# Optimization experiments

Hardware: AMD Instinct MI355X
Metric: run time of the kernel (lower is better)

The kernel has to match this reference:

```python
import math
import jax, jax.numpy as jnp
import numpy as np


def _alibi_slopes(n):
    def pow2_slopes(n):
        start = 2.0 ** (-(2.0 ** (-(math.log2(n) - 3))))
        return [start * (start ** i) for i in range(n)]
    if math.log2(n).is_integer():
        return pow2_slopes(n)
    cp2 = 2 ** math.floor(math.log2(n))
    return pow2_slopes(cp2) + _alibi_slopes(2 * cp2)[0::2][: n - cp2]


NUM_HEADS = 16


def setup_inputs() -> dict:
    key = jax.random.key(0)
    ks = jax.random.split(key, 5)
    B, S, H = 2, 2048, 2048
    return {
        "hidden_states": jax.random.normal(ks[0], (B, S, H), jnp.float32),
        "w_qkv": jax.random.normal(ks[1], (H, 3 * H), jnp.float32) * (H ** -0.5),
        "b_qkv": jax.random.normal(ks[2], (3 * H,), jnp.float32) * 0.02,
        "w_proj": jax.random.normal(ks[3], (H, H), jnp.float32) * (H ** -0.5),
        "b_proj": jax.random.normal(ks[4], (H,), jnp.float32) * 0.02,
    }


def reference(hidden_states, w_qkv, b_qkv, w_proj, b_proj):
    B, S, H = hidden_states.shape
    nh = NUM_HEADS
    hd = H // nh
    scale = 1.0 / hd  # mup scale_qk_dot_by_d=True -> d^-1 (not d^-0.5)

    qkv = hidden_states @ w_qkv + b_qkv  # [B,S,3H]
    q, k, v = jnp.split(qkv, 3, axis=-1)
    q = q.reshape(B, S, nh, hd)
    k = k.reshape(B, S, nh, hd)
    v = v.reshape(B, S, nh, hd)

    scores = jnp.einsum("bqhd,bkhd->bhqk", q, k) * scale  # [B,nh,S,S]

    slopes = jnp.asarray(_alibi_slopes(nh), dtype=scores.dtype)  # [nh]
    pos = jnp.arange(S)
    rel = (pos[None, :] - pos[:, None]).astype(scores.dtype)  # j - i, <=0 in causal region
    bias = slopes[:, None, None] * rel[None, :, :]  # [nh,S,S]
    causal = pos[None, :] <= pos[:, None]  # [S,S]

    scores = jnp.where(causal[None, None], scores + bias[None], jnp.finfo(scores.dtype).min)
    attn = jax.nn.softmax(scores, axis=-1)

    out = jnp.einsum("bhqk,bkhd->bqhd", attn, v).reshape(B, S, H)
    return out @ w_proj + b_proj
```

## Files before the change

### kernel.cpp

```cpp
#include <hip/hip_runtime.h>
#include <hip/hip_bf16.h>

typedef short bf16x8 __attribute__((ext_vector_type(8)));
typedef float f32x4 __attribute__((ext_vector_type(4)));
typedef float f32x16 __attribute__((ext_vector_type(16)));
typedef unsigned short ushort_t;

#define NH 16
#define HD 128
#define SEQ 2048
#define HID 2048
#define NQKV 6144
#define BATCH 2

__device__ __forceinline__ ushort_t f2bf(float x) {
    unsigned u = __builtin_bit_cast(unsigned, x);
    u = (u + 0x7fffu + ((u >> 16) & 1u)) >> 16;
    return (ushort_t)u;
}

__device__ __forceinline__ unsigned cvtpk(float lo, float hi) {
    unsigned r;
    asm("v_cvt_pk_bf16_f32 %0, %1, %2" : "=v"(r) : "v"(lo), "v"(hi));
    return r;
}

__device__ __forceinline__ void gl2lds16(const ushort_t* g, ushort_t* l) {
    __builtin_amdgcn_global_load_lds(
        (__attribute__((address_space(1))) void*)(g),
        (__attribute__((address_space(3))) void*)(l), 16, 0, 0);
}

__global__ __launch_bounds__(256) void prep_fused(
    const float* __restrict__ hidden, ushort_t* __restrict__ hbf,
    const float* __restrict__ wqkv, ushort_t* __restrict__ wqkvT,
    const float* __restrict__ wproj, ushort_t* __restrict__ wprojT) {
    const int bid = blockIdx.x;
    const int t = threadIdx.x;
    if (bid >= 12288 && bid < 16384) {
        int i = (bid - 12288) * 256 + t;
        float4 a0 = *(const float4*)(hidden + (size_t)i * 8);
        float4 a1 = *(const float4*)(hidden + (size_t)i * 8 + 4);
        union { ushort_t u[8]; uint4 v; } p;
        p.u[0]=f2bf(a0.x); p.u[1]=f2bf(a0.y); p.u[2]=f2bf(a0.z); p.u[3]=f2bf(a0.w);
        p.u[4]=f2bf(a1.x); p.u[5]=f2bf(a1.y); p.u[6]=f2bf(a1.z); p.u[7]=f2bf(a1.w);
        *(uint4*)(hbf + (size_t)i * 8) = p.v;
        return;
    }
    const float* w;
    ushort_t* wT;
    int N, bx, by;
    if (bid < 12288) {
        w = wqkv; wT = wqkvT; N = NQKV;
        bx = bid % 192; by = bid / 192;
    } else {
        int b2 = bid - 16384;
        w = wproj; wT = wprojT; N = HID;
        bx = b2 % 64; by = b2 / 64;
    }
    __shared__ float tile[32][33];
    const int nb = bx * 32, kb = by * 32;
    const int tx = t & 31, ty = t >> 5;
#pragma unroll
    for (int i = 0; i < 4; ++i) {
        int k = kb + ty + i * 8;
        tile[ty + i * 8][tx] = w[(size_t)k * N + nb + tx];
    }
    __syncthreads();
#pragma unroll
    for (int i = 0; i < 4; ++i) {
        int n = nb + ty + i * 8;
        wT[(size_t)n * HID + kb + tx] = f2bf(tile[tx][ty + i * 8]);
    }
}

#define GEMM_KLOOP(A_, BT_)                                                     \
    const int t = threadIdx.x;                                                  \
    const int w = t >> 6, lane = t & 63, lm = lane & 15, lq = lane >> 4;        \
    const int wm = (w >> 1) * 64, wn = (w & 1) * 64;                            \
    const int lrow = lane >> 3, lsw = (lane & 7) ^ lrow;                        \
    f32x4 acc[4][4] = {};                                                       \
    const ushort_t* gA = A_ + (size_t)(mb + w * 32 + lrow) * HID + lsw * 8;     \
    const ushort_t* gB = BT_ + (size_t)(nb + w * 32 + lrow) * HID + lsw * 8;    \
    for (int kb = 0; kb < HID; kb += 64) {                                      \
        __syncthreads();                                                        \
        _Pragma("unroll")                                                       \
        for (int c = 0; c < 4; ++c) {                                           \
            gl2lds16(gA + (size_t)c * 8 * HID + kb, At + (w * 256 + c * 64) * 8); \
            gl2lds16(gB + (size_t)c * 8 * HID + kb, Bt + (w * 256 + c * 64) * 8); \
        }                                                                       \
        __syncthreads();                                                        \
        _Pragma("unroll")                                                       \
        for (int kc = 0; kc < 2; ++kc) {                                        \
            const int slot = (kc * 4 + lq) ^ (lm & 7);                          \
            bf16x8 af[4], bfr[4];                                               \
            _Pragma("unroll")                                                   \
            for (int mt = 0; mt < 4; ++mt)                                      \
                af[mt] = ((const bf16x8*)At)[(wm + mt * 16 + lm) * 8 + slot];   \
            _Pragma("unroll")                                                   \
            for (int nt = 0; nt < 4; ++nt)                                      \
                bfr[nt] = ((const bf16x8*)Bt)[(wn + nt * 16 + lm) * 8 + slot];  \
            _Pragma("unroll")                                                   \
            for (int mt = 0; mt < 4; ++mt)                                      \
                _Pragma("unroll")                                               \
                for (int nt = 0; nt < 4; ++nt)                                  \
                    acc[mt][nt] = __builtin_amdgcn_mfma_f32_16x16x32_bf16(      \
                        af[mt], bfr[nt], acc[mt][nt], 0, 0, 0);                 \
        }                                                                       \
    }

__global__ __launch_bounds__(256) void gemm_qkv(
    const ushort_t* __restrict__ A, const ushort_t* __restrict__ BT,
    const float* __restrict__ bias,
    ushort_t* __restrict__ qbuf, ushort_t* __restrict__ kbuf,
    ushort_t* __restrict__ vTbuf) {
    __shared__ unsigned shbuf[128 * 68];
    ushort_t* At = (ushort_t*)shbuf;
    ushort_t* Bt = At + 128 * 64;
    const int mb = blockIdx.x * 128;
    const int nb = blockIdx.y * 128;
    GEMM_KLOOP(A, BT)

    const int sec = nb >> 11;
    if (sec < 2) {
#pragma unroll
        for (int mt = 0; mt < 4; ++mt)
#pragma unroll
            for (int nt = 0; nt < 4; ++nt)
#pragma unroll
                for (int r = 0; r < 4; ++r) {
                    int m = mb + wm + mt * 16 + lq * 4 + r;
                    int c = nb + wn + nt * 16 + lm;
                    float val = acc[mt][nt][r] + bias[c];
                    int h = (c >> 7) & 15;
                    int d = c & 127;
                    int b = m >> 11, s = m & 2047;
                    size_t bh = (size_t)(b * NH + h);
                    ushort_t* dst = (sec == 0) ? qbuf : kbuf;
                    dst[(bh * SEQ + s) * HD + d] = f2bf(val);
                }
    } else {
        __syncthreads();
        unsigned* T = shbuf;
#pragma unroll
        for (int mt = 0; mt < 4; ++mt)
#pragma unroll
            for (int nt = 0; nt < 4; ++nt) {
                const int cl = wn + nt * 16 + lm;
                const int ml = wm + mt * 16 + lq * 4;
                const float bb = bias[nb + cl];
#pragma unroll
                for (int r = 0; r < 4; r += 2) {
                    unsigned pk = (unsigned)f2bf(acc[mt][nt][r] + bb) |
                                  ((unsigned)f2bf(acc[mt][nt][r + 1] + bb) << 16);
                    T[cl * 68 + ((ml + r) >> 1)] = pk;
                }
            }
        __syncthreads();
        const int d = t & 127, sh = t >> 7;
        const int b = mb >> 11, sbase = mb & 2047;
        const int hv = (nb >> 7) - 32;
        ushort_t* vrow = vTbuf + ((size_t)(b * NH + hv) * HD + d) * SEQ + sbase + sh * 64;
#pragma unroll
        for (int i = 0; i < 8; ++i)
            *(uint4*)(vrow + i * 8) = *(const uint4*)&T[d * 68 + sh * 32 + i * 4];
    }
}

__global__ __launch_bounds__(256) void gemm_proj(
    const ushort_t* __restrict__ A, const ushort_t* __restrict__ BT,
    const float* __restrict__ bias, float* __restrict__ out) {
    __shared__ ushort_t Abuf[128 * 64];
    __shared__ ushort_t Bbuf[128 * 64];
    ushort_t* At = Abuf;
    ushort_t* Bt = Bbuf;
    const int mb = blockIdx.x * 128;
    const int nb = blockIdx.y * 128;
    GEMM_KLOOP(A, BT)
#pragma unroll
    for (int mt = 0; mt < 4; ++mt)
#pragma unroll
        for (int nt = 0; nt < 4; ++nt)
#pragma unroll
            for (int r = 0; r < 4; ++r) {
                int m = mb + wm + mt * 16 + lq * 4 + r;
                int c = nb + wn + nt * 16 + lm;
                out[(size_t)m * HID + c] = acc[mt][nt][r] + bias[c];
            }
}

__global__ __launch_bounds__(256) void attn_kernel(
    const ushort_t* __restrict__ qb, const ushort_t* __restrict__ kbuf,
    const ushort_t* __restrict__ vT, ushort_t* __restrict__ ob) {
    __shared__ ushort_t Ks[64 * 128];
    __shared__ ushort_t Vs[128 * 64];

    const int bid = blockIdx.x;
    const int x = bid & 7, g = bid >> 3;
    const int qt = 15 - (g >> 2);
    const int bh = ((g & 3) << 3) | x;
    const int qbase = qt * 128;
    const int t = threadIdx.x, w = t >> 6, lane = t & 63;
    const int l31 = lane & 31, hl = lane >> 5;

    const ushort_t* Qg = qb + (size_t)bh * SEQ * HD;
    const ushort_t* Kg = kbuf + (size_t)bh * SEQ * HD;
    const ushort_t* Vg = vT + (size_t)bh * HD * SEQ;

    const int h = bh & 15;
    const float LOG2E = 1.44269504f;
    const float slope2 = exp2f(-0.5f * (float)(h + 1)) * LOG2E;
    const float scale2 = (1.0f / 128.0f) * LOG2E;

    const int qrow = qbase + w * 32 + l31;
    const int ktd = (qbase + w * 32 + 31) >> 6;

    bf16x8 qf[8];
#pragma unroll
    for (int s = 0; s < 8; ++s) {
        uint4 qv = *(const uint4*)(Qg + (size_t)qrow * HD + (2 * s + hl) * 8);
        qf[s] = __builtin_bit_cast(bf16x8, qv);
    }

    int koffs[4], voffs[4];
#pragma unroll
    for (int i = 0; i < 4; ++i) {
        int ci = i * 256 + t;
        int kr = ci >> 4, ks = ci & 15;
        int kcg = (ks & 8) | ((ks & 7) ^ (kr & 7));
        koffs[i] = kr * HD + kcg * 8;
        int vr = ci >> 3, vs = ci & 7;
        int vcg = vs ^ (vr & 7);
        voffs[i] = vr * SEQ + vcg * 8;
    }

    float mrow = -1e30f, lrow = 0.0f;
    f32x16 O[4] = {};
    const int nkt = 2 * qt + 2;

    for (int kt = 0; kt < nkt; ++kt) {
        __syncthreads();
        {
            const ushort_t* Kt_ = Kg + (size_t)kt * 64 * HD;
            const ushort_t* Vt_ = Vg + (size_t)kt * 64;
#pragma unroll
            for (int i = 0; i < 4; ++i) {
                gl2lds16(Kt_ + koffs[i], Ks + (i * 256 + w * 64) * 8);
                gl2lds16(Vt_ + voffs[i], Vs + (i * 256 + w * 64) * 8);
            }
        }
        __syncthreads();

        if (kt > ktd) continue;

        f32x16 s0 = {}, s1 = {};
        __builtin_amdgcn_s_setprio(1);
#pragma unroll
        for (int s = 0; s < 8; ++s) {
            const int c = 2 * s + hl;
            const int slot = (c & 8) | ((c & 7) ^ (l31 & 7));
            bf16x8 k0 = *(const bf16x8*)&Ks[(l31 * 16 + slot) * 8];
            bf16x8 k1 = *(const bf16x8*)&Ks[((32 + l31) * 16 + slot) * 8];
            s0 = __builtin_amdgcn_mfma_f32_32x32x16_bf16(k0, qf[s], s0, 0, 0, 0);
            s1 = __builtin_amdgcn_mfma_f32_32x32x16_bf16(k1, qf[s], s1, 0, 0, 0);
        }
        __builtin_amdgcn_s_setprio(0);

        const float sb = slope2 * (float)(kt * 64 + 4 * hl - qrow);
        float tm = -3e38f;
        if (kt == ktd) {
#pragma unroll
            for (int r = 0; r < 16; ++r) {
                const int Cr = (r & 3) + 8 * (r >> 2);
                float v0 = s0[r] * scale2 + (sb + slope2 * (float)Cr);
                float v1 = s1[r] * scale2 + (sb + slope2 * (float)(Cr + 32));
                int k0i = kt * 64 + Cr + 4 * hl;
                v0 = (k0i <= qrow) ? v0 : -3e38f;
                v1 = (k0i + 32 <= qrow) ? v1 : -3e38f;
                s0[r] = v0; s1[r] = v1;
                tm = fmaxf(tm, fmaxf(v0, v1));
            }
        } else {
#pragma unroll
            for (int r = 0; r < 16; ++r) {
                const int Cr = (r & 3) + 8 * (r >> 2);
                float v0 = s0[r] * scale2 + (sb + slope2 * (float)Cr);
                float v1 = s1[r] * scale2 + (sb + slope2 * (float)(Cr + 32));
                s0[r] = v0; s1[r] = v1;
                tm = fmaxf(tm, fmaxf(v0, v1));
            }
        }
        tm = fmaxf(tm, __shfl_xor(tm, 32));

        const bool noresc = __all(tm <= mrow + 8.0f) && (kt > 0);
        float mnew, alpha;
        if (noresc) { mnew = mrow; alpha = 1.0f; }
        else { mnew = fmaxf(mrow, tm); alpha = __builtin_amdgcn_exp2f(mrow - mnew); }
        mrow = mnew;

        float psum = 0.0f;
#pragma unroll
        for (int r = 0; r < 16; ++r) {
            float p0 = __builtin_amdgcn_exp2f(s0[r] - mnew);
            float p1 = __builtin_amdgcn_exp2f(s1[r] - mnew);
            s0[r] = p0; s1[r] = p1;
            psum += p0 + p1;
        }
        psum += __shfl_xor(psum, 32);
        lrow = lrow * alpha + psum;

        if (!noresc) {
#pragma unroll
            for (int dt = 0; dt < 4; ++dt)
#pragma unroll
                for (int r = 0; r < 16; ++r) O[dt][r] *= alpha;
        }

        unsigned c0[8], c1[8];
#pragma unroll
        for (int G = 0; G < 4; ++G) {
            c0[G]     = cvtpk(s0[4 * G + 0], s0[4 * G + 1]);
            c1[G]     = cvtpk(s0[4 * G + 2], s0[4 * G + 3]);
            c0[4 + G] = cvtpk(s1[4 * G + 0], s1[4 * G + 1]);
            c1[4 + G] = cvtpk(s1[4 * G + 2], s1[4 * G + 3]);
        }

        __builtin_amdgcn_s_setprio(1);
#pragma unroll
        for (int ks = 0; ks < 4; ++ks) {
            unsigned a0 = c0[2 * ks], a1 = c1[2 * ks];
            unsigned b0 = c0[2 * ks + 1], b1 = c1[2 * ks + 1];
            unsigned own0 = hl ? b0 : a0, own1 = hl ? b1 : a1;
            unsigned snd0 = hl ? a0 : b0, snd1 = hl ? a1 : b1;
            unsigned rcv0 = __shfl_xor(snd0, 32);
            unsigned rcv1 = __shfl_xor(snd1, 32);
            union { unsigned u[4]; bf16x8 v; } pf;
            pf.u[0] = hl ? rcv0 : own0;
            pf.u[1] = hl ? rcv1 : own1;
            pf.u[2] = hl ? own0 : rcv0;
            pf.u[3] = hl ? own1 : rcv1;
            const int c = 2 * ks + hl;
#pragma unroll
            for (int dt = 0; dt < 4; ++dt) {
                const int vr = dt * 32 + l31;
                const int slot = c ^ (vr & 7);
                bf16x8 vf = *(const bf16x8*)&Vs[(vr * 8 + slot) * 8];
                O[dt] = __builtin_amdgcn_mfma_f32_32x32x16_bf16(vf, pf.v, O[dt], 0, 0, 0);
            }
        }
        __builtin_amdgcn_s_setprio(0);
    }

    const float lb = __builtin_amdgcn_rcpf(lrow);
    const int b = bh >> 4;
    ushort_t* orow = ob + ((size_t)(b * SEQ + qrow)) * HID + h * HD;
#pragma unroll
    for (int dt = 0; dt < 4; ++dt)
#pragma unroll
        for (int g4 = 0; g4 < 4; ++g4) {
            union { ushort_t u[4]; uint2 v; } pk;
            pk.u[0] = f2bf(O[dt][4 * g4 + 0] * lb);
            pk.u[1] = f2bf(O[dt][4 * g4 + 1] * lb);
            pk.u[2] = f2bf(O[dt][4 * g4 + 2] * lb);
            pk.u[3] = f2bf(O[dt][4 * g4 + 3] * lb);
            *(uint2*)(orow + dt * 32 + 8 * g4 + 4 * hl) = pk.v;
        }
}

extern "C" void kernel_launch(void* const* d_in, const int* in_sizes, int n_in,
                              void* d_out, int out_size, void* d_ws, size_t ws_size,
                              hipStream_t stream) {
    const float* hidden = (const float*)d_in[0];
    const float* w_qkv = (const float*)d_in[1];
    const float* b_qkv = (const float*)d_in[2];
    const float* w_proj = (const float*)d_in[3];
    const float* b_proj = (const float*)d_in[4];
    float* out = (float*)d_out;

    char* ws = (char*)d_ws;
    size_t off = 0;
    ushort_t* wqkvT = (ushort_t*)(ws + off); off += (size_t)NQKV * HID * 2;
    ushort_t* wprojT = (ushort_t*)(ws + off); off += (size_t)HID * HID * 2;
    ushort_t* hbf = (ushort_t*)(ws + off); off += (size_t)BATCH * SEQ * HID * 2;
    ushort_t* qw = (ushort_t*)(ws + off); off += (size_t)BATCH * NH * SEQ * HD * 2;
    ushort_t* kw = (ushort_t*)(ws + off); off += (size_t)BATCH * NH * SEQ * HD * 2;
    ushort_t* vTw = (ushort_t*)(ws + off); off += (size_t)BATCH * NH * SEQ * HD * 2;
    ushort_t* attnw = (ushort_t*)(ws + off); off += (size_t)BATCH * SEQ * HID * 2;

    prep_fused<<<dim3(20480), 256, 0, stream>>>(
        hidden, hbf, w_qkv, wqkvT, w_proj, wprojT);

    gemm_qkv<<<dim3(BATCH * SEQ / 128, NQKV / 128), 256, 0, stream>>>(
        hbf, wqkvT, b_qkv, qw, kw, vTw);

    attn_kernel<<<dim3(BATCH * NH * 16), 256, 0, stream>>>(qw, kw, vTw, attnw);

    gemm_proj<<<dim3(BATCH * SEQ / 128, HID / 128), 256, 0, stream>>>(
        attnw, wprojT, b_proj, out);
}
```

Before: 368.6 us.

## Double-buffer K/V tiles in attention kernel to overlap loads with compute

Adds two LDS buffers each for the K and V tiles and prefetches tile kt+1 into the idle buffer while tile kt is computed. Partial vmcnt waits keep the next tile's global-to-LDS copies in flight during compute. This hides load latency behind the MFMA work. In exchange LDS use doubles from 32KB to 64KB per block, which may lower occupancy.

```diff
diff --git a/kernel.cpp b/kernel.cpp
--- a/kernel.cpp
+++ b/kernel.cpp
@@ -192,8 +192,8 @@
 __global__ __launch_bounds__(256) void attn_kernel(
     const ushort_t* __restrict__ qb, const ushort_t* __restrict__ kbuf,
     const ushort_t* __restrict__ vT, ushort_t* __restrict__ ob) {
-    __shared__ ushort_t Ks[64 * 128];
-    __shared__ ushort_t Vs[128 * 64];
+    __shared__ ushort_t Ks[2][64 * 128];
+    __shared__ ushort_t Vs[2][128 * 64];
 
     const int bid = blockIdx.x;
     const int x = bid & 7, g = bid >> 3;
@@ -234,22 +234,34 @@
         voffs[i] = vr * SEQ + vcg * 8;
     }
 
+#define ATTN_STAGE(KT, BUF)                                                   \
+    {                                                                         \
+        const ushort_t* Kt_ = Kg + (size_t)(KT) * 64 * HD;                    \
+        const ushort_t* Vt_ = Vg + (size_t)(KT) * 64;                         \
+        _Pragma("unroll")                                                     \
+        for (int i = 0; i < 4; ++i) {                                         \
+            gl2lds16(Kt_ + koffs[i], Ks[BUF] + (i * 256 + w * 64) * 8);       \
+            gl2lds16(Vt_ + voffs[i], Vs[BUF] + (i * 256 + w * 64) * 8);       \
+        }                                                                     \
+    }
+
     float mrow = -1e30f, lrow = 0.0f;
     f32x16 O[4] = {};
     const int nkt = 2 * qt + 2;
 
+    ATTN_STAGE(0, 0)
+
     for (int kt = 0; kt < nkt; ++kt) {
-        __syncthreads();
-        {
-            const ushort_t* Kt_ = Kg + (size_t)kt * 64 * HD;
-            const ushort_t* Vt_ = Vg + (size_t)kt * 64;
-#pragma unroll
-            for (int i = 0; i < 4; ++i) {
-                gl2lds16(Kt_ + koffs[i], Ks + (i * 256 + w * 64) * 8);
-                gl2lds16(Vt_ + voffs[i], Vs + (i * 256 + w * 64) * 8);
-            }
-        }
-        __syncthreads();
+        const int cur = kt & 1;
+        __builtin_amdgcn_s_barrier();
+        if (kt + 1 < nkt) {
+            ATTN_STAGE(kt + 1, cur ^ 1)
+            asm volatile("s_waitcnt vmcnt(8)" ::: "memory");
+        } else {
+            asm volatile("s_waitcnt vmcnt(0)" ::: "memory");
+        }
+        __builtin_amdgcn_s_barrier();
+        __builtin_amdgcn_sched_barrier(0);
 
         if (kt > ktd) continue;
 
@@ -259,8 +271,8 @@
         for (int s = 0; s < 8; ++s) {
             const int c = 2 * s + hl;
             const int slot = (c & 8) | ((c & 7) ^ (l31 & 7));
-            bf16x8 k0 = *(const bf16x8*)&Ks[(l31 * 16 + slot) * 8];
-            bf16x8 k1 = *(const bf16x8*)&Ks[((32 + l31) * 16 + slot) * 8];
+            bf16x8 k0 = *(const bf16x8*)&Ks[cur][(l31 * 16 + slot) * 8];
+            bf16x8 k1 = *(const bf16x8*)&Ks[cur][((32 + l31) * 16 + slot) * 8];
             s0 = __builtin_amdgcn_mfma_f32_32x32x16_bf16(k0, qf[s], s0, 0, 0, 0);
             s1 = __builtin_amdgcn_mfma_f32_32x32x16_bf16(k1, qf[s], s1, 0, 0, 0);
         }
@@ -344,7 +356,7 @@
             for (int dt = 0; dt < 4; ++dt) {
                 const int vr = dt * 32 + l31;
                 const int slot = c ^ (vr & 7);
-                bf16x8 vf = *(const bf16x8*)&Vs[(vr * 8 + slot) * 8];
+                bf16x8 vf = *(const bf16x8*)&Vs[cur][(vr * 8 + slot) * 8];
                 O[dt] = __builtin_amdgcn_mfma_f32_32x32x16_bf16(vf, pf.v, O[dt], 0, 0, 0);
             }
         }
@@ -365,6 +377,7 @@
             pk.u[3] = f2bf(O[dt][4 * g4 + 3] * lb);
             *(uint2*)(orow + dt * 32 + 8 * g4 + 4 * hl) = pk.v;
         }
+#undef ATTN_STAGE
 }
 
 extern "C" void kernel_launch(void* const* d_in, const int* in_sizes, int n_in,
```

Measured after the change: 371.0 us. No clear change (+0.6%).

## Move w_proj transpose into attention kernel tail and reorder query tiles

Applied to the files above, without the earlier changes.

The w_proj fp32-to-bf16 transpose moves out of the prep kernel and runs as extra blocks appended to the attention launch. These cheap blocks can fill compute units that sit idle during the attention's load-imbalanced tail, and the prep kernel shrinks. The query-tile ordering also changes: the first half of the grid issues long causal tiles in descending order and the second half issues short tiles in ascending order, to improve load balance. The cost is some added branching in the attention kernel, and the transpose reuses the K shared-memory buffer as its tile.

```diff
diff --git a/kernel.cpp b/kernel.cpp
--- a/kernel.cpp
+++ b/kernel.cpp
@@ -33,11 +33,10 @@
 
 __global__ __launch_bounds__(256) void prep_fused(
     const float* __restrict__ hidden, ushort_t* __restrict__ hbf,
-    const float* __restrict__ wqkv, ushort_t* __restrict__ wqkvT,
-    const float* __restrict__ wproj, ushort_t* __restrict__ wprojT) {
+    const float* __restrict__ wqkv, ushort_t* __restrict__ wqkvT) {
     const int bid = blockIdx.x;
     const int t = threadIdx.x;
-    if (bid >= 12288 && bid < 16384) {
+    if (bid >= 12288) {
         int i = (bid - 12288) * 256 + t;
         float4 a0 = *(const float4*)(hidden + (size_t)i * 8);
         float4 a1 = *(const float4*)(hidden + (size_t)i * 8 + 4);
@@ -47,30 +46,20 @@
         *(uint4*)(hbf + (size_t)i * 8) = p.v;
         return;
     }
-    const float* w;
-    ushort_t* wT;
-    int N, bx, by;
-    if (bid < 12288) {
-        w = wqkv; wT = wqkvT; N = NQKV;
-        bx = bid % 192; by = bid / 192;
-    } else {
-        int b2 = bid - 16384;
-        w = wproj; wT = wprojT; N = HID;
-        bx = b2 % 64; by = b2 / 64;
-    }
+    const int bx = bid % 192, by = bid / 192;
     __shared__ float tile[32][33];
     const int nb = bx * 32, kb = by * 32;
     const int tx = t & 31, ty = t >> 5;
 #pragma unroll
     for (int i = 0; i < 4; ++i) {
         int k = kb + ty + i * 8;
-        tile[ty + i * 8][tx] = w[(size_t)k * N + nb + tx];
+        tile[ty + i * 8][tx] = wqkv[(size_t)k * NQKV + nb + tx];
     }
     __syncthreads();
 #pragma unroll
     for (int i = 0; i < 4; ++i) {
         int n = nb + ty + i * 8;
-        wT[(size_t)n * HID + kb + tx] = f2bf(tile[tx][ty + i * 8]);
+        wqkvT[(size_t)n * HID + kb + tx] = f2bf(tile[tx][ty + i * 8]);
     }
 }
 
@@ -189,18 +178,42 @@
             }
 }
 
-__global__ __launch_bounds__(256) void attn_kernel(
+__global__ __launch_bounds__(256) void attn_fused(
     const ushort_t* __restrict__ qb, const ushort_t* __restrict__ kbuf,
-    const ushort_t* __restrict__ vT, ushort_t* __restrict__ ob) {
+    const ushort_t* __restrict__ vT, ushort_t* __restrict__ ob,
+    const float* __restrict__ wproj, ushort_t* __restrict__ wprojT) {
     __shared__ ushort_t Ks[64 * 128];
     __shared__ ushort_t Vs[128 * 64];
 
     const int bid = blockIdx.x;
-    const int x = bid & 7, g = bid >> 3;
-    const int qt = 15 - (g >> 2);
-    const int bh = ((g & 3) << 3) | x;
+    const int t = threadIdx.x;
+
+    if (bid >= 512) {
+        float* tile = (float*)Ks;
+        const int b2 = bid - 512;
+        const int bx = b2 & 63, by = b2 >> 6;
+        const int nb = bx * 32, kb = by * 32;
+        const int tx = t & 31, ty = t >> 5;
+#pragma unroll
+        for (int i = 0; i < 4; ++i) {
+            int k = kb + ty + i * 8;
+            tile[(ty + i * 8) * 33 + tx] = wproj[(size_t)k * HID + nb + tx];
+        }
+        __syncthreads();
+#pragma unroll
+        for (int i = 0; i < 4; ++i) {
+            int n = nb + ty + i * 8;
+            wprojT[(size_t)n * HID + kb + tx] = f2bf(tile[tx * 33 + ty + i * 8]);
+        }
+        return;
+    }
+
+    const int x = bid & 7, j = bid >> 3;
+    const int hi = j & 3, m = j >> 2;
+    const int qt = (m < 8) ? (15 - m) : (m - 8);
+    const int bh = (hi << 3) | x;
     const int qbase = qt * 128;
-    const int t = threadIdx.x, w = t >> 6, lane = t & 63;
+    const int w = t >> 6, lane = t & 63;
     const int l31 = lane & 31, hl = lane >> 5;
 
     const ushort_t* Qg = qb + (size_t)bh * SEQ * HD;
@@ -387,13 +400,13 @@
     ushort_t* vTw = (ushort_t*)(ws + off); off += (size_t)BATCH * NH * SEQ * HD * 2;
     ushort_t* attnw = (ushort_t*)(ws + off); off += (size_t)BATCH * SEQ * HID * 2;
 
-    prep_fused<<<dim3(20480), 256, 0, stream>>>(
-        hidden, hbf, w_qkv, wqkvT, w_proj, wprojT);
+    prep_fused<<<dim3(16384), 256, 0, stream>>>(hidden, hbf, w_qkv, wqkvT);
 
     gemm_qkv<<<dim3(BATCH * SEQ / 128, NQKV / 128), 256, 0, stream>>>(
         hbf, wqkvT, b_qkv, qw, kw, vTw);
 
-    attn_kernel<<<dim3(BATCH * NH * 16), 256, 0, stream>>>(qw, kw, vTw, attnw);
+    attn_fused<<<dim3(512 + 4096), 256, 0, stream>>>(
+        qw, kw, vTw, attnw, w_proj, wprojT);
 
     gemm_proj<<<dim3(BATCH * SEQ / 128, HID / 128), 256, 0, stream>>>(
         attnw, wprojT, b_proj, out);
```

Measured after the change: 377.2 us. 1.02x slower.
